# Kernel tuning notes

Hardware: AMD Instinct MI355X
Metric: run time of the kernel (lower is better)

Reference implementation:

```python
import jax, jax.numpy as jnp
import numpy as np

N = 20000   # nodes
E = 320000  # edges
H = 4       # attention heads
GAT_SLOPE = 0.2   # DGL GATv2Conv internal leaky_relu slope
ACT_SLOPE = 0.01  # nn.LeakyReLU default slope


def gatv2_layer(h, src, dst, Wl, Wr, attn, b):
    """DGL GATv2Conv (share_weights=False, bias=True, eval mode).
    h: [N, Fin]; Wl/Wr: [Fin, H*D]; attn: [H, D]; b: [H*D]. Returns [N, H, D]."""
    n = h.shape[0]
    Hh, D = attn.shape
    fs = (h @ Wl).reshape(n, Hh, D)  # source projection
    fd = (h @ Wr).reshape(n, Hh, D)  # destination projection
    # edge-wise GATv2 score: a^T leaky_relu(Wl h_u + Wr h_v)
    e = jax.nn.leaky_relu(fs[src] + fd[dst], negative_slope=GAT_SLOPE)  # [E,H,D]
    logit = jnp.einsum('ehd,hd->eh', e, attn)  # [E,H]
    # edge softmax over incoming edges of each dst node (numerically stable)
    m = jax.ops.segment_max(logit, dst, num_segments=n)
    a = jnp.exp(logit - m[dst])
    s = jax.ops.segment_sum(a, dst, num_segments=n)
    alpha = a / s[dst]  # [E,H]
    out = jax.ops.segment_sum(alpha[:, :, None] * fs[src], dst, num_segments=n)
    return out + b.reshape(1, Hh, D)


def setup_inputs() -> dict:
    key = jax.random.key(0)
    ks = jax.random.split(key, 16)

    def w(k, shape, fan_in):
        return (jax.random.normal(k, shape, jnp.float32) / np.float32(np.sqrt(fan_in)))

    return {
        'n_feat': jax.random.normal(ks[0], (N, 512), jnp.float32),
        'src': jax.random.randint(ks[1], (E,), 0, N, jnp.int32),
        'dst': jax.random.randint(ks[2], (E,), 0, N, jnp.int32),
        # layer 0: 512 -> H x 128
        'Wl0': w(ks[3], (512, H * 128), 512), 'Wr0': w(ks[4], (512, H * 128), 512),
        'attn0': w(ks[5], (H, 128), 128), 'b0': jnp.zeros((H * 128,), jnp.float32),
        # layer 1: 128 -> H x 128
        'Wl1': w(ks[6], (128, H * 128), 128), 'Wr1': w(ks[7], (128, H * 128), 128),
        'attn1': w(ks[8], (H, 128), 128), 'b1': jnp.zeros((H * 128,), jnp.float32),
        # layer 2 (output): 128 -> H x 64
        'Wl2': w(ks[9], (128, H * 64), 128), 'Wr2': w(ks[10], (128, H * 64), 128),
        'attn2': w(ks[11], (H, 64), 64), 'b2': jnp.zeros((H * 64,), jnp.float32),
    }


def reference(n_feat, src, dst, Wl0, Wr0, attn0, b0, Wl1, Wr1, attn1, b1,
              Wl2, Wr2, attn2, b2):
    h = n_feat.reshape(n_feat.shape[0], -1)  # nn.Flatten
    for (Wl, Wr, attn, b) in ((Wl0, Wr0, attn0, b0),
                              (Wl1, Wr1, attn1, b1),
                              (Wl2, Wr2, attn2, b2)):
        h = gatv2_layer(h, src, dst, Wl, Wr, attn, b)  # [N,H,D]
        h = h.mean(axis=1)                              # head mean
        h = jax.nn.leaky_relu(h, negative_slope=ACT_SLOPE)
    # dgl.mean_nodes: per-graph mean readout (single graph -> [1, out])
    return h.mean(axis=0, keepdims=True)
```

## Files before the change

### kernel.cpp

```cpp
#include <hip/hip_runtime.h>
#include <hip/hip_bf16.h>
#include <stdint.h>


#define GAT_SLOPE 0.2f
#define ACT_SLOPE 0.01f
#define MAXDEG 64

typedef _Float16 half8 __attribute__((ext_vector_type(8)));
typedef _Float16 v2h __attribute__((ext_vector_type(2)));
typedef float floatx4 __attribute__((ext_vector_type(4)));

struct TransDesc {
  const float* src;
  _Float16* dst;
  int K, M, off;
};
struct PreArgs {
  TransDesc d[9];
  int wTotal;
  const float* nf;
  _Float16* A0;
  int aTotal;
  const int* src;
  const int* dst;
  int* counts;
  int* pcsrc;
  int E;
};

__global__ __launch_bounds__(256) void preproc_kernel(PreArgs pa) {
  int i = blockIdx.x * 256 + threadIdx.x;
  const int total = pa.wTotal + pa.aTotal + pa.E;
  if (i >= total) return;
  if (i < pa.wTotal) {
    int q = 0;
#pragma unroll
    for (int j = 1; j < 9; ++j)
      if (i >= pa.d[j].off) q = j;
    int local = i - pa.d[q].off;
    int K = pa.d[q].K, M = pa.d[q].M;
    int m = local / K, k = local % K;
    pa.d[q].dst[local] = (_Float16)pa.d[q].src[(size_t)k * M + m];
  } else if (i < pa.wTotal + pa.aTotal) {
    int j = i - pa.wTotal;
    pa.A0[j] = (_Float16)pa.nf[j];
  } else {
    int e = i - pa.wTotal - pa.aTotal;
    int d = pa.dst[e];
    int pos = atomicAdd(&pa.counts[d], 1);
    if (pos < MAXDEG) pa.pcsrc[(size_t)d * MAXDEG + pos] = pa.src[e];
  }
}

__device__ __forceinline__ void gload_lds16(const _Float16* g, _Float16* l) {
  __builtin_amdgcn_global_load_lds(
      (__attribute__((address_space(1))) unsigned int*)g,
      (__attribute__((address_space(3))) unsigned int*)l, 16, 0, 0);
}

#define TM 128
#define TN 128
#define TK 32

__global__ __launch_bounds__(256) void gemm_mfma_dual_kernel(
    const _Float16* __restrict__ A, const _Float16* __restrict__ B0,
    const _Float16* __restrict__ B1, _Float16* __restrict__ C0,
    _Float16* __restrict__ C1, int Nrow, int K, int M, int nStrips,
    int nbxLog2) {
  const int id = blockIdx.x;
  const int xcd = id & 7;
  const int s = id >> 3;
  const int nbx = 1 << nbxLog2;
  const int col = s & (nbx - 1);
  const int chunk = s >> nbxLog2;
  const int strip = chunk * 8 + xcd;
  if (strip >= nStrips) return;

  const int nb = nbx >> 1;
  const bool second = col >= nb;
  const _Float16* B = second ? B1 : B0;
  _Float16* C = second ? C1 : C0;
  const int bn = (second ? col - nb : col) * TN;
  const int bm = strip * TM;

  __shared__ __align__(16) _Float16 As[TM * TK];
  __shared__ __align__(16) _Float16 Bs[TN * TK];

  const int tid = threadIdx.x;
  const int w = tid >> 6;
  const int lane = tid & 63;
  const int wr = w >> 1;
  const int wc = w & 1;
  const int quad = lane >> 4;
  const int lr = lane & 15;

  const int lrow = lane >> 2;
  const int loff = (lane & 3) * 8;

  floatx4 acc[4][4];
#pragma unroll
  for (int i = 0; i < 4; ++i)
#pragma unroll
    for (int j = 0; j < 4; ++j) acc[i][j] = (floatx4){0.f, 0.f, 0.f, 0.f};

  const int KT = K / TK;
  for (int kt = 0; kt < KT; ++kt) {
    const int k0 = kt * TK;
#pragma unroll
    for (int half = 0; half < 2; ++half) {
      const int r0 = w * 32 + half * 16;
      int ga = bm + r0 + lrow;
      if (ga >= Nrow) ga = Nrow - 1;
      gload_lds16(A + (size_t)ga * K + k0 + loff, As + r0 * TK);
      gload_lds16(B + (size_t)(bn + r0 + lrow) * K + k0 + loff, Bs + r0 * TK);
    }
    __syncthreads();

    half8 ar[4], br[4];
#pragma unroll
    for (int i = 0; i < 4; ++i) {
      int row = wr * 64 + i * 16 + lr;
      ar[i] = *(const half8*)(As + row * TK + quad * 8);
    }
#pragma unroll
    for (int j = 0; j < 4; ++j) {
      int colr = wc * 64 + j * 16 + lr;
      br[j] = *(const half8*)(Bs + colr * TK + quad * 8);
    }
#pragma unroll
    for (int i = 0; i < 4; ++i)
#pragma unroll
      for (int j = 0; j < 4; ++j)
        acc[i][j] = __builtin_amdgcn_mfma_f32_16x16x32_f16(ar[i], br[j],
                                                           acc[i][j], 0, 0, 0);
    __syncthreads();
  }

#pragma unroll
  for (int i = 0; i < 4; ++i) {
#pragma unroll
    for (int r = 0; r < 4; ++r) {
      int row = bm + wr * 64 + i * 16 + quad * 4 + r;
      if (row >= Nrow) continue;
#pragma unroll
      for (int j = 0; j < 4; ++j) {
        int colc = bn + wc * 64 + j * 16 + lr;
        C[(size_t)row * M + colc] = (_Float16)acc[i][j][r];
      }
    }
  }
}

template <int CTRL>
__device__ __forceinline__ float dpp_add(float x) {
  int y = __builtin_amdgcn_update_dpp(0, __builtin_bit_cast(int, x), CTRL,
                                      0xF, 0xF, true);
  return x + __builtin_bit_cast(float, y);
}
__device__ __forceinline__ float row_sum16(float x) {
  x = dpp_add<0x121>(x);
  x = dpp_add<0x122>(x);
  x = dpp_add<0x124>(x);
  x = dpp_add<0x128>(x);
  return x;
}

template <int D>
__global__ __launch_bounds__(128) void node_attn_kernel(
    const _Float16* __restrict__ fs, const _Float16* __restrict__ fd,
    const int* __restrict__ counts, const int* __restrict__ pcsrc,
    const _Float16* __restrict__ attnT, const float* __restrict__ bias,
    float* __restrict__ hout, _Float16* __restrict__ oh, int N) {
  constexpr int HD = 4 * D;
  constexpr int R = HD / 64;
  constexpr int R2 = R / 2;
  typedef _Float16 halfR __attribute__((ext_vector_type(R)));
  union Frag {
    halfR v;
    v2h h[R2];
    _Float16 s[R];
  };
  const int wid = threadIdx.x >> 6;
  const int lane = threadIdx.x & 63;

  __shared__ float sO[2][64 * R];
  __shared__ float sML[2][2][64];

  const v2h slope2 = {(_Float16)GAT_SLOPE, (_Float16)GAT_SLOPE};
  Frag arf;
  arf.v = *(const halfR*)(attnT + lane * R);

  int vcur = blockIdx.x;
  int cnt_c = 0, idx_c = 0;
  Frag fdv_c;
  if (vcur < N) {
    cnt_c = min(counts[vcur], MAXDEG);
    idx_c = pcsrc[(size_t)vcur * MAXDEG + lane];
    fdv_c.v = *(const halfR*)(fd + (size_t)vcur * HD + lane * R);
  }

  int parity = 0;
  for (int v = blockIdx.x; v < N; v += gridDim.x, parity ^= 1) {
    const int vn = v + gridDim.x;
    int cnt_n = 0, idx_n = 0;
    Frag fdv_n;
    if (vn < N) {
      cnt_n = min(counts[vn], MAXDEG);
      idx_n = pcsrc[(size_t)vn * MAXDEG + lane];
      fdv_n.v = *(const halfR*)(fd + (size_t)vn * HD + lane * R);
    }

    const int cnt = cnt_c;
    const int idxv = idx_c;
    const Frag fdvl = fdv_c;

    float m = -INFINITY, l = 0.f;
    float O[R];
#pragma unroll
    for (int i = 0; i < R; ++i) O[i] = 0.f;

    const int mid = (cnt + 1) >> 1;
    int k = wid ? mid : 0;
    const int ke = wid ? cnt : mid;

    auto loadb = [&](Frag* t, int kk) {
#pragma unroll
      for (int q = 0; q < 4; ++q) {
        const int sidx = __builtin_amdgcn_readlane(idxv, kk + q);
        t[q].v = *(const halfR*)(fs + (size_t)sidx * HD + lane * R);
      }
    };

    auto compute4 = [&](Frag* t) {
      float p0 = 0.f, p1 = 0.f, p2 = 0.f, p3 = 0.f;
#pragma unroll
      for (int j = 0; j < R2; ++j) {
        v2h x0 = t[0].h[j] + fdvl.h[j];
        v2h x1 = t[1].h[j] + fdvl.h[j];
        v2h x2 = t[2].h[j] + fdvl.h[j];
        v2h x3 = t[3].h[j] + fdvl.h[j];
        x0 = __builtin_elementwise_max(x0, x0 * slope2);
        x1 = __builtin_elementwise_max(x1, x1 * slope2);
        x2 = __builtin_elementwise_max(x2, x2 * slope2);
        x3 = __builtin_elementwise_max(x3, x3 * slope2);
        p0 = __builtin_amdgcn_fdot2(arf.h[j], x0, p0, false);
        p1 = __builtin_amdgcn_fdot2(arf.h[j], x1, p1, false);
        p2 = __builtin_amdgcn_fdot2(arf.h[j], x2, p2, false);
        p3 = __builtin_amdgcn_fdot2(arf.h[j], x3, p3, false);
      }
      p0 = row_sum16(p0);
      p1 = row_sum16(p1);
      p2 = row_sum16(p2);
      p3 = row_sum16(p3);
      const float mq = fmaxf(fmaxf(p0, p1), fmaxf(p2, p3));
      const float mnew = fmaxf(m, mq);
      const float sc = __expf(m - mnew);
      const float w0 = __expf(p0 - mnew);
      const float w1 = __expf(p1 - mnew);
      const float w2 = __expf(p2 - mnew);
      const float w3 = __expf(p3 - mnew);
      l = l * sc + (w0 + w1 + w2 + w3);
#pragma unroll
      for (int i = 0; i < R; ++i) {
        float acc = (float)t[0].s[i] * w0;
        acc = fmaf((float)t[1].s[i], w1, acc);
        acc = fmaf((float)t[2].s[i], w2, acc);
        acc = fmaf((float)t[3].s[i], w3, acc);
        O[i] = fmaf(O[i], sc, acc);
      }
      m = mnew;
    };

    {
      const int nb = (ke - k) >> 2;
      if (nb > 0) {
        Frag tA[4], tB[4];
        loadb(tA, k);
        int bi = 0;
        for (;;) {
          if (bi + 1 < nb) loadb(tB, k + 4);
          compute4(tA);
          k += 4;
          ++bi;
          if (bi == nb) break;
          if (bi + 1 < nb) loadb(tA, k + 4);
          compute4(tB);
          k += 4;
          ++bi;
          if (bi == nb) break;
        }
      }
    }
    for (; k < ke; ++k) {
      const int sidx = __builtin_amdgcn_readlane(idxv, k);
      Frag t0;
      t0.v = *(const halfR*)(fs + (size_t)sidx * HD + lane * R);
      float p0 = 0.f;
#pragma unroll
      for (int j = 0; j < R2; ++j) {
        v2h x0 = t0.h[j] + fdvl.h[j];
        x0 = __builtin_elementwise_max(x0, x0 * slope2);
        p0 = __builtin_amdgcn_fdot2(arf.h[j], x0, p0, false);
      }
      p0 = row_sum16(p0);
      const float mnew = fmaxf(m, p0);
      const float sc = __expf(m - mnew);
      const float p = __expf(p0 - mnew);
      l = l * sc + p;
#pragma unroll
      for (int i = 0; i < R; ++i) O[i] = fmaf(O[i], sc, p * (float)t0.s[i]);
      m = mnew;
    }

    if (wid == 1) {
      sML[parity][0][lane] = m;
      sML[parity][1][lane] = l;
#pragma unroll
      for (int i = 0; i < R; ++i) sO[parity][i * 64 + lane] = O[i];
    }
    __syncthreads();
    if (wid == 0) {
      const float m1 = sML[parity][0][lane];
      const float l1 = sML[parity][1][lane];
      const float mstar = fmaxf(m, m1);
      const float a0 = (l > 0.f) ? __expf(m - mstar) : 0.f;
      const float a1 = (l1 > 0.f) ? __expf(m1 - mstar) : 0.f;
      l = l * a0 + l1 * a1;
#pragma unroll
      for (int i = 0; i < R; ++i) O[i] = O[i] * a0 + sO[parity][i * 64 + lane] * a1;

      const float inv = (l > 0.f) ? 1.f / l : 0.f;
      float biasv[R];
#pragma unroll
      for (int i = 0; i < R; i += 4) {
        floatx4 b4 = *(const floatx4*)(bias + lane * R + i);
        biasv[i] = b4[0];
        biasv[i + 1] = b4[1];
        biasv[i + 2] = b4[2];
        biasv[i + 3] = b4[3];
      }
#pragma unroll
      for (int i = 0; i < R; ++i) O[i] = O[i] * inv + biasv[i];
#pragma unroll
      for (int i = 0; i < R; ++i) {
        O[i] += __shfl_xor(O[i], 16, 64);
        O[i] += __shfl_xor(O[i], 32, 64);
        float x = O[i] * 0.25f;
        O[i] = x > 0.f ? x : x * ACT_SLOPE;
      }
      if (lane < 16) {
        const size_t base = (size_t)v * D + lane * R;
        if (hout) {
#pragma unroll
          for (int i = 0; i < R; ++i) hout[base + i] = O[i];
        }
        if (oh) {
#pragma unroll
          for (int i = 0; i < R; ++i) oh[base + i] = (_Float16)O[i];
        }
      }
    }
    cnt_c = cnt_n;
    idx_c = idx_n;
    fdv_c = fdv_n;
  }
}

__global__ __launch_bounds__(64) void final_mean_kernel(
    const float* __restrict__ h, float* __restrict__ out, int N) {
  const int d = threadIdx.x;
  float acc = 0.f;
  for (int n = blockIdx.x; n < N; n += gridDim.x) acc += h[(size_t)n * 64 + d];
  atomicAdd(&out[d], acc / (float)N);
}

extern "C" void kernel_launch(void* const* d_in, const int* in_sizes, int n_in,
                              void* d_out, int out_size, void* d_ws,
                              size_t ws_size, hipStream_t stream) {
  const float* n_feat = (const float*)d_in[0];
  const int* src = (const int*)d_in[1];
  const int* dst = (const int*)d_in[2];
  const float* Wl[3] = {(const float*)d_in[3], (const float*)d_in[7],
                        (const float*)d_in[11]};
  const float* Wr[3] = {(const float*)d_in[4], (const float*)d_in[8],
                        (const float*)d_in[12]};
  const float* attn[3] = {(const float*)d_in[5], (const float*)d_in[9],
                          (const float*)d_in[13]};
  const float* bias[3] = {(const float*)d_in[6], (const float*)d_in[10],
                          (const float*)d_in[14]};

  const int N = in_sizes[0] / 512;
  const int E = in_sizes[1];
  const int Kdim[3] = {512, 128, 128};
  const int Mdim[3] = {512, 512, 256};
  const int attnLen[3] = {512, 512, 256};

  char* ws = (char*)d_ws;
  size_t o = 0;
  auto alloc = [&](size_t bytes) {
    void* p = ws + o;
    o += (bytes + 15) & ~(size_t)15;
    return p;
  };
  _Float16* fs = (_Float16*)alloc((size_t)N * 512 * 2);
  _Float16* fd = (_Float16*)alloc((size_t)N * 512 * 2);
  _Float16* A0 = (_Float16*)alloc((size_t)N * 512 * 2);
  _Float16* h1 = (_Float16*)alloc((size_t)N * 128 * 2);
  _Float16* h2 = (_Float16*)alloc((size_t)N * 128 * 2);
  float* hfin = (float*)alloc((size_t)N * 64 * 4);
  _Float16 *WlT[3], *WrT[3], *attnT[3];
  for (int L = 0; L < 3; ++L) {
    size_t sz = (size_t)Kdim[L] * Mdim[L] * 2;
    WlT[L] = (_Float16*)alloc(sz);
    WrT[L] = (_Float16*)alloc(sz);
  }
  for (int L = 0; L < 3; ++L) attnT[L] = (_Float16*)alloc(attnLen[L] * 2);
  int* counts = (int*)alloc((size_t)N * 4);
  int* pcsrc = (int*)alloc((size_t)N * MAXDEG * 4);

  hipMemsetAsync(counts, 0, (size_t)N * sizeof(int), stream);
  {
    PreArgs pa;
    int off = 0;
    for (int L = 0; L < 3; ++L) {
      pa.d[2 * L] = {Wl[L], WlT[L], Kdim[L], Mdim[L], off};
      off += Kdim[L] * Mdim[L];
      pa.d[2 * L + 1] = {Wr[L], WrT[L], Kdim[L], Mdim[L], off};
      off += Kdim[L] * Mdim[L];
    }
    for (int L = 0; L < 3; ++L) {
      pa.d[6 + L] = {attn[L], attnT[L], attnLen[L], 1, off};
      off += attnLen[L];
    }
    pa.wTotal = off;
    pa.nf = n_feat;
    pa.A0 = A0;
    pa.aTotal = N * 512;
    pa.src = src;
    pa.dst = dst;
    pa.counts = counts;
    pa.pcsrc = pcsrc;
    pa.E = E;
    int total = pa.wTotal + pa.aTotal + pa.E;
    preproc_kernel<<<(total + 255) / 256, 256, 0, stream>>>(pa);
  }

  const _Float16* Ain[3] = {A0, h1, h2};

  const int nStrips = (N + TM - 1) / TM;
  const int S8 = ((nStrips + 7) / 8) * 8;

  const int attnGrid = (N + 7) / 8;

  for (int L = 0; L < 3; ++L) {
    const int K = Kdim[L], M = Mdim[L];
    const int nbx = 2 * M / TN;
    const int nbxLog2 = (nbx == 8) ? 3 : 2;
    gemm_mfma_dual_kernel<<<S8 * nbx, 256, 0, stream>>>(
        Ain[L], WlT[L], WrT[L], fs, fd, N, K, M, nStrips, nbxLog2);
    if (L == 0) {
      node_attn_kernel<128><<<attnGrid, 128, 0, stream>>>(
          fs, fd, counts, pcsrc, attnT[L], bias[L], nullptr, h1, N);
    } else if (L == 1) {
      node_attn_kernel<128><<<attnGrid, 128, 0, stream>>>(
          fs, fd, counts, pcsrc, attnT[L], bias[L], nullptr, h2, N);
    } else {
      node_attn_kernel<64><<<attnGrid, 128, 0, stream>>>(
          fs, fd, counts, pcsrc, attnT[L], bias[L], hfin, nullptr, N);
    }
  }

  hipMemsetAsync(d_out, 0, 64 * sizeof(float), stream);
  final_mean_kernel<<<256, 64, 0, stream>>>(hfin, (float*)d_out, N);
}
```

Baseline: 366.9 us.

## Launch one block per node and fold log2e into attention weights for exp2

Replaces the persistent grid-stride node loop, which prefetched the next node's metadata and used double-buffered shared memory, with one block per destination node (grid = N). Attention vectors are pre-scaled by log2(e) during preprocessing so the online softmax can use the hardware exp2 directly instead of expf. The aim is more blocks in flight to hide gather latency and cheaper exponentials. In exchange it drops the cross-node prefetch and pays more block launch overhead, and the log2e factor is rounded into fp16 attention weights.

```diff
diff --git a/kernel.cpp b/kernel.cpp
--- a/kernel.cpp
+++ b/kernel.cpp
@@ -6,6 +6,7 @@
 #define GAT_SLOPE 0.2f
 #define ACT_SLOPE 0.01f
 #define MAXDEG 64
+#define LOG2E 1.44269504088896340736f
 
 typedef _Float16 half8 __attribute__((ext_vector_type(8)));
 typedef _Float16 v2h __attribute__((ext_vector_type(2)));
@@ -15,6 +16,7 @@
   const float* src;
   _Float16* dst;
   int K, M, off;
+  float scale;
 };
 struct PreArgs {
   TransDesc d[9];
@@ -41,7 +43,8 @@
     int local = i - pa.d[q].off;
     int K = pa.d[q].K, M = pa.d[q].M;
     int m = local / K, k = local % K;
-    pa.d[q].dst[local] = (_Float16)pa.d[q].src[(size_t)k * M + m];
+    pa.d[q].dst[local] =
+        (_Float16)(pa.d[q].src[(size_t)k * M + m] * pa.d[q].scale);
   } else if (i < pa.wTotal + pa.aTotal) {
     int j = i - pa.wTotal;
     pa.A0[j] = (_Float16)pa.nf[j];
@@ -181,189 +184,169 @@
     v2h h[R2];
     _Float16 s[R];
   };
+  const int v = blockIdx.x;
+  if (v >= N) return;
   const int wid = threadIdx.x >> 6;
   const int lane = threadIdx.x & 63;
 
-  __shared__ float sO[2][64 * R];
-  __shared__ float sML[2][2][64];
-
   const v2h slope2 = {(_Float16)GAT_SLOPE, (_Float16)GAT_SLOPE};
+
+  const int cnt = min(counts[v], MAXDEG);
+  int idxReg = pcsrc[(size_t)v * MAXDEG + lane];
+  Frag fdv;
+  fdv.v = *(const halfR*)(fd + (size_t)v * HD + lane * R);
   Frag arf;
   arf.v = *(const halfR*)(attnT + lane * R);
 
-  int vcur = blockIdx.x;
-  int cnt_c = 0, idx_c = 0;
-  Frag fdv_c;
-  if (vcur < N) {
-    cnt_c = min(counts[vcur], MAXDEG);
-    idx_c = pcsrc[(size_t)vcur * MAXDEG + lane];
-    fdv_c.v = *(const halfR*)(fd + (size_t)vcur * HD + lane * R);
-  }
-
-  int parity = 0;
-  for (int v = blockIdx.x; v < N; v += gridDim.x, parity ^= 1) {
-    const int vn = v + gridDim.x;
-    int cnt_n = 0, idx_n = 0;
-    Frag fdv_n;
-    if (vn < N) {
-      cnt_n = min(counts[vn], MAXDEG);
-      idx_n = pcsrc[(size_t)vn * MAXDEG + lane];
-      fdv_n.v = *(const halfR*)(fd + (size_t)vn * HD + lane * R);
-    }
-
-    const int cnt = cnt_c;
-    const int idxv = idx_c;
-    const Frag fdvl = fdv_c;
-
-    float m = -INFINITY, l = 0.f;
-    float O[R];
-#pragma unroll
-    for (int i = 0; i < R; ++i) O[i] = 0.f;
-
-    const int mid = (cnt + 1) >> 1;
-    int k = wid ? mid : 0;
-    const int ke = wid ? cnt : mid;
-
-    auto loadb = [&](Frag* t, int kk) {
-#pragma unroll
-      for (int q = 0; q < 4; ++q) {
-        const int sidx = __builtin_amdgcn_readlane(idxv, kk + q);
-        t[q].v = *(const halfR*)(fs + (size_t)sidx * HD + lane * R);
+  float m = -INFINITY, l = 0.f;
+  float O[R];
+#pragma unroll
+  for (int i = 0; i < R; ++i) O[i] = 0.f;
+
+  const int mid = (cnt + 1) >> 1;
+  int k = wid ? mid : 0;
+  const int ke = wid ? cnt : mid;
+
+  auto loadb = [&](Frag* t, int kk) {
+#pragma unroll
+    for (int q = 0; q < 4; ++q) {
+      const int sidx = __builtin_amdgcn_readlane(idxReg, kk + q);
+      t[q].v = *(const halfR*)(fs + (size_t)sidx * HD + lane * R);
+    }
+  };
+
+  auto compute4 = [&](Frag* t) {
+    float p0 = 0.f, p1 = 0.f, p2 = 0.f, p3 = 0.f;
+#pragma unroll
+    for (int j = 0; j < R2; ++j) {
+      v2h x0 = t[0].h[j] + fdv.h[j];
+      v2h x1 = t[1].h[j] + fdv.h[j];
+      v2h x2 = t[2].h[j] + fdv.h[j];
+      v2h x3 = t[3].h[j] + fdv.h[j];
+      x0 = __builtin_elementwise_max(x0, x0 * slope2);
+      x1 = __builtin_elementwise_max(x1, x1 * slope2);
+      x2 = __builtin_elementwise_max(x2, x2 * slope2);
+      x3 = __builtin_elementwise_max(x3, x3 * slope2);
+      p0 = __builtin_amdgcn_fdot2(arf.h[j], x0, p0, false);
+      p1 = __builtin_amdgcn_fdot2(arf.h[j], x1, p1, false);
+      p2 = __builtin_amdgcn_fdot2(arf.h[j], x2, p2, false);
+      p3 = __builtin_amdgcn_fdot2(arf.h[j], x3, p3, false);
+    }
+    p0 = row_sum16(p0);
+    p1 = row_sum16(p1);
+    p2 = row_sum16(p2);
+    p3 = row_sum16(p3);
+    const float mq = fmaxf(fmaxf(p0, p1), fmaxf(p2, p3));
+    const float mnew = fmaxf(m, mq);
+    const float sc = __builtin_amdgcn_exp2f(m - mnew);
+    const float w0 = __builtin_amdgcn_exp2f(p0 - mnew);
+    const float w1 = __builtin_amdgcn_exp2f(p1 - mnew);
+    const float w2 = __builtin_amdgcn_exp2f(p2 - mnew);
+    const float w3 = __builtin_amdgcn_exp2f(p3 - mnew);
+    l = l * sc + (w0 + w1 + w2 + w3);
+#pragma unroll
+    for (int i = 0; i < R; ++i) {
+      float acc = (float)t[0].s[i] * w0;
+      acc = fmaf((float)t[1].s[i], w1, acc);
+      acc = fmaf((float)t[2].s[i], w2, acc);
+      acc = fmaf((float)t[3].s[i], w3, acc);
+      O[i] = fmaf(O[i], sc, acc);
+    }
+    m = mnew;
+  };
+
+  {
+    const int nb = (ke - k) >> 2;
+    if (nb > 0) {
+      Frag tA[4], tB[4];
+      loadb(tA, k);
+      int bi = 0;
+      for (;;) {
+        if (bi + 1 < nb) loadb(tB, k + 4);
+        compute4(tA);
+        k += 4;
+        ++bi;
+        if (bi == nb) break;
+        if (bi + 1 < nb) loadb(tA, k + 4);
+        compute4(tB);
+        k += 4;
+        ++bi;
+        if (bi == nb) break;
       }
-    };
-
-    auto compute4 = [&](Frag* t) {
-      float p0 = 0.f, p1 = 0.f, p2 = 0.f, p3 = 0.f;
-#pragma unroll
-      for (int j = 0; j < R2; ++j) {
-        v2h x0 = t[0].h[j] + fdvl.h[j];
-        v2h x1 = t[1].h[j] + fdvl.h[j];
-        v2h x2 = t[2].h[j] + fdvl.h[j];
-        v2h x3 = t[3].h[j] + fdvl.h[j];
-        x0 = __builtin_elementwise_max(x0, x0 * slope2);
-        x1 = __builtin_elementwise_max(x1, x1 * slope2);
-        x2 = __builtin_elementwise_max(x2, x2 * slope2);
-        x3 = __builtin_elementwise_max(x3, x3 * slope2);
-        p0 = __builtin_amdgcn_fdot2(arf.h[j], x0, p0, false);
-        p1 = __builtin_amdgcn_fdot2(arf.h[j], x1, p1, false);
-        p2 = __builtin_amdgcn_fdot2(arf.h[j], x2, p2, false);
-        p3 = __builtin_amdgcn_fdot2(arf.h[j], x3, p3, false);
-      }
-      p0 = row_sum16(p0);
-      p1 = row_sum16(p1);
-      p2 = row_sum16(p2);
-      p3 = row_sum16(p3);
-      const float mq = fmaxf(fmaxf(p0, p1), fmaxf(p2, p3));
-      const float mnew = fmaxf(m, mq);
-      const float sc = __expf(m - mnew);
-      const float w0 = __expf(p0 - mnew);
-      const float w1 = __expf(p1 - mnew);
-      const float w2 = __expf(p2 - mnew);
-      const float w3 = __expf(p3 - mnew);
-      l = l * sc + (w0 + w1 + w2 + w3);
-#pragma unroll
-      for (int i = 0; i < R; ++i) {
-        float acc = (float)t[0].s[i] * w0;
-        acc = fmaf((float)t[1].s[i], w1, acc);
-        acc = fmaf((float)t[2].s[i], w2, acc);
-        acc = fmaf((float)t[3].s[i], w3, acc);
-        O[i] = fmaf(O[i], sc, acc);
-      }
-      m = mnew;
-    };
-
-    {
-      const int nb = (ke - k) >> 2;
-      if (nb > 0) {
-        Frag tA[4], tB[4];
-        loadb(tA, k);
-        int bi = 0;
-        for (;;) {
-          if (bi + 1 < nb) loadb(tB, k + 4);
-          compute4(tA);
-          k += 4;
-          ++bi;
-          if (bi == nb) break;
-          if (bi + 1 < nb) loadb(tA, k + 4);
-          compute4(tB);
-          k += 4;
-          ++bi;
-          if (bi == nb) break;
-        }
-      }
-    }
-    for (; k < ke; ++k) {
-      const int sidx = __builtin_amdgcn_readlane(idxv, k);
-      Frag t0;
-      t0.v = *(const halfR*)(fs + (size_t)sidx * HD + lane * R);
-      float p0 = 0.f;
-#pragma unroll
-      for (int j = 0; j < R2; ++j) {
-        v2h x0 = t0.h[j] + fdvl.h[j];
-        x0 = __builtin_elementwise_max(x0, x0 * slope2);
-        p0 = __builtin_amdgcn_fdot2(arf.h[j], x0, p0, false);
-      }
-      p0 = row_sum16(p0);
-      const float mnew = fmaxf(m, p0);
-      const float sc = __expf(m - mnew);
-      const float p = __expf(p0 - mnew);
-      l = l * sc + p;
-#pragma unroll
-      for (int i = 0; i < R; ++i) O[i] = fmaf(O[i], sc, p * (float)t0.s[i]);
-      m = mnew;
-    }
-
-    if (wid == 1) {
-      sML[parity][0][lane] = m;
-      sML[parity][1][lane] = l;
-#pragma unroll
-      for (int i = 0; i < R; ++i) sO[parity][i * 64 + lane] = O[i];
-    }
-    __syncthreads();
-    if (wid == 0) {
-      const float m1 = sML[parity][0][lane];
-      const float l1 = sML[parity][1][lane];
-      const float mstar = fmaxf(m, m1);
-      const float a0 = (l > 0.f) ? __expf(m - mstar) : 0.f;
-      const float a1 = (l1 > 0.f) ? __expf(m1 - mstar) : 0.f;
-      l = l * a0 + l1 * a1;
-#pragma unroll
-      for (int i = 0; i < R; ++i) O[i] = O[i] * a0 + sO[parity][i * 64 + lane] * a1;
-
-      const float inv = (l > 0.f) ? 1.f / l : 0.f;
-      float biasv[R];
-#pragma unroll
-      for (int i = 0; i < R; i += 4) {
-        floatx4 b4 = *(const floatx4*)(bias + lane * R + i);
-        biasv[i] = b4[0];
-        biasv[i + 1] = b4[1];
-        biasv[i + 2] = b4[2];
-        biasv[i + 3] = b4[3];
-      }
-#pragma unroll
-      for (int i = 0; i < R; ++i) O[i] = O[i] * inv + biasv[i];
-#pragma unroll
-      for (int i = 0; i < R; ++i) {
-        O[i] += __shfl_xor(O[i], 16, 64);
-        O[i] += __shfl_xor(O[i], 32, 64);
-        float x = O[i] * 0.25f;
-        O[i] = x > 0.f ? x : x * ACT_SLOPE;
-      }
-      if (lane < 16) {
-        const size_t base = (size_t)v * D + lane * R;
-        if (hout) {
-#pragma unroll
-          for (int i = 0; i < R; ++i) hout[base + i] = O[i];
-        }
-        if (oh) {
-#pragma unroll
-          for (int i = 0; i < R; ++i) oh[base + i] = (_Float16)O[i];
-        }
-      }
-    }
-    cnt_c = cnt_n;
-    idx_c = idx_n;
-    fdv_c = fdv_n;
+    }
+  }
+  for (; k < ke; ++k) {
+    const int sidx = __builtin_amdgcn_readlane(idxReg, k);
+    Frag t0;
+    t0.v = *(const halfR*)(fs + (size_t)sidx * HD + lane * R);
+    float p0 = 0.f;
+#pragma unroll
+    for (int j = 0; j < R2; ++j) {
+      v2h x0 = t0.h[j] + fdv.h[j];
+      x0 = __builtin_elementwise_max(x0, x0 * slope2);
+      p0 = __builtin_amdgcn_fdot2(arf.h[j], x0, p0, false);
+    }
+    p0 = row_sum16(p0);
+    const float mnew = fmaxf(m, p0);
+    const float sc = __builtin_amdgcn_exp2f(m - mnew);
+    const float p = __builtin_amdgcn_exp2f(p0 - mnew);
+    l = l * sc + p;
+#pragma unroll
+    for (int i = 0; i < R; ++i) O[i] = fmaf(O[i], sc, p * (float)t0.s[i]);
+    m = mnew;
+  }
+
+  __shared__ float sO[64 * R];
+  __shared__ float sM[64];
+  __shared__ float sL[64];
+  if (wid == 1) {
+    sM[lane] = m;
+    sL[lane] = l;
+#pragma unroll
+    for (int i = 0; i < R; ++i) sO[i * 64 + lane] = O[i];
+  }
+  __syncthreads();
+  if (wid == 1) return;
+  {
+    const float m1 = sM[lane];
+    const float l1 = sL[lane];
+    const float mstar = fmaxf(m, m1);
+    const float a0 = (l > 0.f) ? __builtin_amdgcn_exp2f(m - mstar) : 0.f;
+    const float a1 = (l1 > 0.f) ? __builtin_amdgcn_exp2f(m1 - mstar) : 0.f;
+    l = l * a0 + l1 * a1;
+#pragma unroll
+    for (int i = 0; i < R; ++i) O[i] = O[i] * a0 + sO[i * 64 + lane] * a1;
+  }
+
+  const float inv = (l > 0.f) ? 1.f / l : 0.f;
+  float biasv[R];
+#pragma unroll
+  for (int i = 0; i < R; i += 4) {
+    floatx4 b4 = *(const floatx4*)(bias + lane * R + i);
+    biasv[i] = b4[0];
+    biasv[i + 1] = b4[1];
+    biasv[i + 2] = b4[2];
+    biasv[i + 3] = b4[3];
+  }
+#pragma unroll
+  for (int i = 0; i < R; ++i) O[i] = O[i] * inv + biasv[i];
+#pragma unroll
+  for (int i = 0; i < R; ++i) {
+    O[i] += __shfl_xor(O[i], 16, 64);
+    O[i] += __shfl_xor(O[i], 32, 64);
+    float x = O[i] * 0.25f;
+    O[i] = x > 0.f ? x : x * ACT_SLOPE;
+  }
+  if (lane < 16) {
+    const size_t base = (size_t)v * D + lane * R;
+    if (hout) {
+#pragma unroll
+      for (int i = 0; i < R; ++i) hout[base + i] = O[i];
+    }
+    if (oh) {
+#pragma unroll
+      for (int i = 0; i < R; ++i) oh[base + i] = (_Float16)O[i];
+    }
   }
 }
 
@@ -424,13 +407,13 @@
     PreArgs pa;
     int off = 0;
     for (int L = 0; L < 3; ++L) {
-      pa.d[2 * L] = {Wl[L], WlT[L], Kdim[L], Mdim[L], off};
+      pa.d[2 * L] = {Wl[L], WlT[L], Kdim[L], Mdim[L], off, 1.f};
       off += Kdim[L] * Mdim[L];
-      pa.d[2 * L + 1] = {Wr[L], WrT[L], Kdim[L], Mdim[L], off};
+      pa.d[2 * L + 1] = {Wr[L], WrT[L], Kdim[L], Mdim[L], off, 1.f};
       off += Kdim[L] * Mdim[L];
     }
     for (int L = 0; L < 3; ++L) {
-      pa.d[6 + L] = {attn[L], attnT[L], attnLen[L], 1, off};
+      pa.d[6 + L] = {attn[L], attnT[L], attnLen[L], 1, off, LOG2E};
       off += attnLen[L];
     }
     pa.wTotal = off;
@@ -451,8 +434,6 @@
   const int nStrips = (N + TM - 1) / TM;
   const int S8 = ((nStrips + 7) / 8) * 8;
 
-  const int attnGrid = (N + 7) / 8;
-
   for (int L = 0; L < 3; ++L) {
     const int K = Kdim[L], M = Mdim[L];
     const int nbx = 2 * M / TN;
@@ -460,14 +441,17 @@
     gemm_mfma_dual_kernel<<<S8 * nbx, 256, 0, stream>>>(
         Ain[L], WlT[L], WrT[L], fs, fd, N, K, M, nStrips, nbxLog2);
     if (L == 0) {
-      node_attn_kernel<128><<<attnGrid, 128, 0, stream>>>(
-          fs, fd, counts, pcsrc, attnT[L], bias[L], nullptr, h1, N);
+      node_attn_kernel<128><<<N, 128, 0, stream>>>(fs, fd, counts, pcsrc,
+                                                   attnT[L], bias[L], nullptr,
+                                                   h1, N);
     } else if (L == 1) {
-      node_attn_kernel<128><<<attnGrid, 128, 0, stream>>>(
-          fs, fd, counts, pcsrc, attnT[L], bias[L], nullptr, h2, N);
+      node_attn_kernel<128><<<N, 128, 0, stream>>>(fs, fd, counts, pcsrc,
+                                                   attnT[L], bias[L], nullptr,
+                                                   h2, N);
     } else {
-      node_attn_kernel<64><<<attnGrid, 128, 0, stream>>>(
-          fs, fd, counts, pcsrc, attnT[L], bias[L], hfin, nullptr, N);
+      node_attn_kernel<64><<<N, 128, 0, stream>>>(fs, fd, counts, pcsrc,
+                                                  attnT[L], bias[L], hfin,
+                                                  nullptr, N);
     }
   }
 
```

New measurement: 344.4 us. 1.07x faster.
